# Optimization experiments

Measured on AMD Instinct MI355X. Metric: run time of the kernel, lower is better.

The kernel has to match this reference:

```python
import jax, jax.numpy as jnp
import numpy as np

K = 20
NEG_SLOPE = 0.2


def knn_idx(x, k):
    # squared euclidean pairwise distances [N, N]
    sq = jnp.sum(x * x, axis=-1)
    d = sq[:, None] - 2.0 * (x @ x.T) + sq[None, :]
    _, idx = jax.lax.top_k(-d, k)  # k nearest (self included, dist 0)
    return idx  # [N, k]


def edge_conv(x, W, b, k):
    # Dynamic EdgeConv: kNN on current features, gather, concat[x_i, x_j - x_i], MLP, max over neighbors
    idx = knn_idx(x, k)                 # [N, k]
    xj = x[idx]                         # [N, k, C] gather
    xi = jnp.broadcast_to(x[:, None, :], xj.shape)
    e = jnp.concatenate([xi, xj - xi], axis=-1)   # [N, k, 2C]
    h = jax.nn.leaky_relu(jnp.einsum('nkc,cf->nkf', e, W) + b, NEG_SLOPE)
    return jnp.max(h, axis=1)           # [N, F] max-aggregation


def setup_inputs() -> dict:
    key = jax.random.key(0)
    ks = jax.random.split(key, 7)
    N, C_in, H, F_out = 16384, 3, 64, 128
    def lin(k1, k2, fan_in, fan_out):
        lim = 1.0 / np.sqrt(fan_in)
        W = jax.random.uniform(k1, (fan_in, fan_out), jnp.float32, -lim, lim)
        b = jax.random.uniform(k2, (fan_out,), jnp.float32, -lim, lim)
        return W, b
    x = jax.random.normal(ks[0], (N, C_in), jnp.float32)
    W1, b1 = lin(ks[1], ks[2], 2 * C_in, H)
    W2, b2 = lin(ks[3], ks[4], 2 * H, H)
    W3, b3 = lin(ks[5], ks[6], 2 * H, F_out)
    return {"x": x, "W1": W1, "b1": b1, "W2": W2, "b2": b2, "W3": W3, "b3": b3}


def reference(x, W1, b1, W2, b2, W3, b3):
    h = edge_conv(x, W1, b1, K)
    h = edge_conv(h, W2, b2, K)
    h = edge_conv(h, W3, b3, K)
    return h
```

## Files before the change

kernel.cpp:

```cpp
#include <hip/hip_runtime.h>
#include <math.h>

#define K_NN 20
#define NEG_SLOPE 0.2f

constexpr int NSEG = 8;
constexpr int BKT  = 16;
constexpr int OCAP = 6144;

__device__ __forceinline__ void insert_sorted(float (&dl)[K_NN], int (&il)[K_NN],
                                              float d, int idx) {
    if (d < dl[K_NN - 1]) {
        dl[K_NN - 1] = d; il[K_NN - 1] = idx;
#pragma unroll
        for (int p = K_NN - 1; p > 0; --p) {
            if (dl[p] < dl[p - 1]) {
                float td = dl[p]; dl[p] = dl[p - 1]; dl[p - 1] = td;
                int   ti = il[p]; il[p] = il[p - 1]; il[p - 1] = ti;
            }
        }
    }
}

template<int C>
__global__ __launch_bounds__(256) void sqnorm_kernel(const float* __restrict__ x,
                                                     float* __restrict__ sq, int N) {
    int i = blockIdx.x * 256 + threadIdx.x;
    if (i < N) {
        float s = 0.f;
#pragma unroll
        for (int c = 0; c < C; ++c) { float v = x[i * C + c]; s += v * v; }
        sq[i] = s;
    }
}

__global__ __launch_bounds__(256) void pack3_kernel(const float* __restrict__ x,
                                                    float4* __restrict__ x4, int N) {
    int i = blockIdx.x * 256 + threadIdx.x;
    if (i < N) {
        float a = x[i * 3], b = x[i * 3 + 1], c = x[i * 3 + 2];
        float s = a * a; s += b * b; s += c * c;
        x4[i] = make_float4(a, b, c, s);
    }
}

__global__ __launch_bounds__(128) void tau3_kernel(const float4* __restrict__ x4,
                                                   float* __restrict__ tau, int N) {
    __shared__ float bufD[16 * 128];
    __shared__ int   bufI[16 * 128];
    const int tid = threadIdx.x;
    const int q   = blockIdx.x * 128 + tid;
    const float4 qv = x4[q];

    float dl[K_NN]; int il[K_NN];
#pragma unroll
    for (int p = 0; p < K_NN; ++p) { dl[p] = __builtin_inff(); il[p] = 0; }
    int cnt = 0;

    for (int j0 = 0; j0 < 2048; j0 += 8) {
#pragma unroll
        for (int u = 0; u < 8; ++u) {
            float4 pv = x4[j0 + u];
            float dot = qv.x * pv.x; dot += qv.y * pv.y; dot += qv.z * pv.z;
            float d = (qv.w - 2.f * dot) + pv.w;
            if (d < dl[K_NN - 1]) { bufD[tid + 128 * cnt] = d; bufI[tid + 128 * cnt] = j0 + u; ++cnt; }
        }
        if (__any(cnt >= 8)) {
            for (int u2 = 0; u2 < cnt; ++u2)
                insert_sorted(dl, il, bufD[tid + 128 * u2], bufI[tid + 128 * u2]);
            cnt = 0;
        }
    }
    for (int u2 = 0; u2 < cnt; ++u2)
        insert_sorted(dl, il, bufD[tid + 128 * u2], bufI[tid + 128 * u2]);

    tau[q] = dl[K_NN - 1] * 1.000002f + 2e-6f * qv.w;
}

__global__ __launch_bounds__(256) void knn3w_kernel(const float4* __restrict__ x4,
                                                    const float* __restrict__ tau,
                                                    float* __restrict__ pdist,
                                                    int* __restrict__ pidx, int N) {
    __shared__ float4 tile4[128];
    __shared__ float bufD[16 * 256];
    __shared__ int   bufI[16 * 256];
    const int tid = threadIdx.x;
    const int q   = blockIdx.x * 256 + tid;
    const int seg = blockIdx.y;
    const int segLen = N / NSEG;
    const int j0  = seg * segLen;

    const float4 qv = x4[q];
    const float  tq = tau[q];

    float dl[K_NN]; int il[K_NN];
#pragma unroll
    for (int p = 0; p < K_NN; ++p) { dl[p] = __builtin_inff(); il[p] = 0; }
    int cnt = 0;

    for (int t0 = 0; t0 < segLen; t0 += 128) {
        __syncthreads();
        if (tid < 128) tile4[tid] = x4[j0 + t0 + tid];
        __syncthreads();
        for (int jj = 0; jj < 128; jj += 8) {
#pragma unroll
            for (int u = 0; u < 8; ++u) {
                float4 pv = tile4[jj + u];
                float dot = qv.x * pv.x; dot += qv.y * pv.y; dot += qv.z * pv.z;
                float d = (qv.w - 2.f * dot) + pv.w;
                if (d <= tq && d < dl[K_NN - 1]) {
                    bufD[tid + 256 * cnt] = d;
                    bufI[tid + 256 * cnt] = j0 + t0 + jj + u;
                    ++cnt;
                }
            }
            if (__any(cnt >= 8)) {
                for (int u2 = 0; u2 < cnt; ++u2)
                    insert_sorted(dl, il, bufD[tid + 256 * u2], bufI[tid + 256 * u2]);
                cnt = 0;
            }
        }
    }
    for (int u2 = 0; u2 < cnt; ++u2)
        insert_sorted(dl, il, bufD[tid + 256 * u2], bufI[tid + 256 * u2]);

    const size_t base = ((size_t)q * NSEG + seg) * K_NN;
#pragma unroll
    for (int p = 0; p < K_NN; ++p) { pdist[base + p] = dl[p]; pidx[base + p] = il[p]; }
}

__global__ __launch_bounds__(256) void tau64_kernel(const float* __restrict__ feat,
                                                    const float* __restrict__ sq,
                                                    const int* __restrict__ knn,
                                                    float* __restrict__ tau, int N) {
    int q = blockIdx.x * 256 + threadIdx.x;
    if (q >= N) return;
    const float4* qrow = (const float4*)&feat[(size_t)q * 64];
    float4 qf[16];
#pragma unroll
    for (int m = 0; m < 16; ++m) qf[m] = qrow[m];
    const float qsq = sq[q];
    float t = 0.f;
    for (int k = 0; k < K_NN; ++k) {
        int j = knn[(size_t)q * K_NN + k];
        const float4* prow = (const float4*)&feat[(size_t)j * 64];
        float dot = 0.f;
#pragma unroll
        for (int m = 0; m < 16; ++m) {
            float4 pv = prow[m];
            dot += qf[m].x * pv.x; dot += qf[m].y * pv.y;
            dot += qf[m].z * pv.z; dot += qf[m].w * pv.w;
        }
        float d = (qsq - 2.f * dot) + sq[j];
        t = fmaxf(t, d);
    }
    tau[q] = t * 1.000002f + 2e-6f * qsq;
}

__global__ __launch_bounds__(256) void transpose64_kernel(const float* __restrict__ xin,
                                                          float* __restrict__ xT, int N) {
    int i = blockIdx.x * 256 + threadIdx.x;
    int c = blockIdx.y;
    xT[(size_t)c * N + i] = xin[(size_t)i * 64 + c];
}

__global__ __launch_bounds__(256, 2) void fused64s_kernel(const float* __restrict__ xT,
                                                          const float* __restrict__ sq,
                                                          const float* __restrict__ tau,
                                                          float* __restrict__ pdist,
                                                          int* __restrict__ pidx,
                                                          uint2* __restrict__ ovG, int N) {
    __shared__ float qT[64][132];
    __shared__ float pTc[2][8][140];
    __shared__ float qbufD[BKT][128];
    __shared__ int   qbufI[BKT][128];
    __shared__ float lstD[K_NN][128];
    __shared__ int   lstI[K_NN][128];
    __shared__ int   qn[128];
    __shared__ float thr_s[128];
    __shared__ int   ovf;
    __shared__ int   ovn;

    const int tid = threadIdx.x;
    const int q0  = blockIdx.x * 128;
    const int seg = blockIdx.y;
    const int segLen = N / NSEG;
    const int j0  = seg * segLen;
    uint2* ovBase = ovG + (size_t)(seg * gridDim.x + blockIdx.x) * OCAP;

    const int qg = tid >> 4, pg = tid & 15;
    const int qcol = qg * 8;
    const int pcol = pg * 8 + 4 * (pg >> 2);

#pragma unroll
    for (int k = 0; k < 8; ++k) {
        int v = tid + 256 * k; int c = v >> 5; int dd = (v & 31) * 4;
        *(float4*)&qT[c][dd] = *(const float4*)&xT[(size_t)c * N + q0 + dd];
    }
    float qsv[8];
    *(float4*)&qsv[0] = *(const float4*)&sq[q0 + qcol];
    *(float4*)&qsv[4] = *(const float4*)&sq[q0 + qcol + 4];
    float qtau[8];
    *(float4*)&qtau[0] = *(const float4*)&tau[q0 + qcol];
    *(float4*)&qtau[4] = *(const float4*)&tau[q0 + qcol + 4];

    if (tid < 128) {
        qn[tid] = 0; thr_s[tid] = __builtin_inff();
#pragma unroll
        for (int p = 0; p < K_NN; ++p) { lstD[p][tid] = __builtin_inff(); lstI[p][tid] = 0x7fffffff; }
    }
    if (tid == 0) { ovf = 0; ovn = 0; }

    const int stc  = tid >> 5;
    const int std_ = (tid & 31) * 4;
    const int sts  = std_ + 4 * (std_ >> 5);

    *(float4*)&pTc[0][stc][sts] = *(const float4*)&xT[(size_t)stc * N + j0 + std_];
    __syncthreads();

    int buf = 0;
    for (int t = 0; t < 16; ++t) {
        const int jb = j0 + t * 128;
        float acc[8][8];
#pragma unroll
        for (int i = 0; i < 8; ++i)
#pragma unroll
            for (int j = 0; j < 8; ++j) acc[i][j] = 0.f;

        for (int cc = 0; cc < 8; ++cc) {
            const bool last = (t == 15) && (cc == 7);
            float4 pnext;
            if (!last) {
                const int ncc = (cc + 1) & 7;
                const int njb = (cc == 7) ? jb + 128 : jb;
                pnext = *(const float4*)&xT[(size_t)(ncc * 8 + stc) * N + njb + std_];
            }
#pragma unroll
            for (int c8 = 0; c8 < 8; ++c8) {
                const int c = cc * 8 + c8;
                float4 qa  = *(const float4*)&qT[c][qcol];
                float4 qb4 = *(const float4*)&qT[c][qcol + 4];
                float4 pa  = *(const float4*)&pTc[buf][c8][pcol];
                float4 pb4 = *(const float4*)&pTc[buf][c8][pcol + 4];
                float qf[8] = {qa.x, qa.y, qa.z, qa.w, qb4.x, qb4.y, qb4.z, qb4.w};
                float pf[8] = {pa.x, pa.y, pa.z, pa.w, pb4.x, pb4.y, pb4.z, pb4.w};
#pragma unroll
                for (int i = 0; i < 8; ++i)
#pragma unroll
                    for (int j = 0; j < 8; ++j) acc[i][j] += qf[i] * pf[j];
            }
            if (!last) *(float4*)&pTc[buf ^ 1][stc][sts] = pnext;
            __syncthreads();
            buf ^= 1;
        }

        float psv[8];
        *(float4*)&psv[0] = *(const float4*)&sq[jb + pg * 8];
        *(float4*)&psv[4] = *(const float4*)&sq[jb + pg * 8 + 4];
        float thr_c[8];
#pragma unroll
        for (int i = 0; i < 8; ++i) thr_c[i] = thr_s[qcol + i];
        const int tbase = t * 128;

#pragma unroll
        for (int i = 0; i < 8; ++i) {
#pragma unroll
            for (int j = 0; j < 8; ++j) {
                float d = (qsv[i] - 2.f * acc[i][j]) + psv[j];
                if (d <= qtau[i] && d < thr_c[i]) {
                    int slot = atomicAdd(&qn[qcol + i], 1);
                    if (slot < BKT) {
                        qbufD[slot][qcol + i] = d;
                        qbufI[slot][qcol + i] = tbase + pg * 8 + j;
                    } else {
                        int os = atomicAdd(&ovn, 1);
                        if (os < OCAP)
                            ovBase[os] = make_uint2(__float_as_uint(d),
                                                    (unsigned)(((qcol + i) << 11) | (tbase + pg * 8 + j)));
                        ovf = 1;
                    }
                }
            }
        }
        __syncthreads();
        const int doDrain = ovf;
        __syncthreads();
        if (doDrain) {
            if (tid < 128) {
                int c = qn[tid]; c = (c < BKT) ? c : BKT;
                for (int s = 0; s < c; ++s) {
                    float d = qbufD[s][tid]; int idx = j0 + qbufI[s][tid];
                    float td = lstD[K_NN - 1][tid]; int ti = lstI[K_NN - 1][tid];
                    if (d < td || (d == td && idx < ti)) {
                        lstD[K_NN - 1][tid] = d; lstI[K_NN - 1][tid] = idx;
#pragma unroll
                        for (int p = K_NN - 1; p > 0; --p) {
                            float a = lstD[p][tid], b = lstD[p - 1][tid];
                            int  ai = lstI[p][tid], bi = lstI[p - 1][tid];
                            if (a < b || (a == b && ai < bi)) {
                                lstD[p][tid] = b; lstD[p - 1][tid] = a;
                                lstI[p][tid] = bi; lstI[p - 1][tid] = ai;
                            } else break;
                        }
                    }
                }
                qn[tid] = 0;
                thr_s[tid] = lstD[K_NN - 1][tid];
            }
            if (tid == 0) ovf = 0;
            __syncthreads();
        }
    }

    if (tid < 128) {
        int c = qn[tid]; c = (c < BKT) ? c : BKT;
        int tot = ovn; tot = (tot < OCAP) ? tot : OCAP;
        for (int s = 0; s < c + tot; ++s) {
            float d; int idx;
            if (s < c) { d = qbufD[s][tid]; idx = j0 + qbufI[s][tid]; }
            else {
                uint2 v = ovBase[s - c];
                if ((int)(v.y >> 11) != tid) continue;
                d = __uint_as_float(v.x); idx = j0 + (int)(v.y & 2047u);
            }
            float td = lstD[K_NN - 1][tid]; int ti = lstI[K_NN - 1][tid];
            if (d < td || (d == td && idx < ti)) {
                lstD[K_NN - 1][tid] = d; lstI[K_NN - 1][tid] = idx;
#pragma unroll
                for (int p = K_NN - 1; p > 0; --p) {
                    float a = lstD[p][tid], b = lstD[p - 1][tid];
                    int  ai = lstI[p][tid], bi = lstI[p - 1][tid];
                    if (a < b || (a == b && ai < bi)) {
                        lstD[p][tid] = b; lstD[p - 1][tid] = a;
                        lstI[p][tid] = bi; lstI[p - 1][tid] = ai;
                    } else break;
                }
            }
        }
        const size_t base = ((size_t)(q0 + tid) * NSEG + seg) * K_NN;
#pragma unroll
        for (int p = 0; p < K_NN; ++p) { pdist[base + p] = lstD[p][tid]; pidx[base + p] = lstI[p][tid]; }
    }
}

__global__ __launch_bounds__(256) void knn_merge_kernel(const float* __restrict__ pdist,
                                                        const int* __restrict__ pidx,
                                                        int* __restrict__ knn, int N) {
    int q = blockIdx.x * 256 + threadIdx.x;
    if (q >= N) return;
    float dl[K_NN]; int il[K_NN];
#pragma unroll
    for (int p = 0; p < K_NN; ++p) { dl[p] = __builtin_inff(); il[p] = 0; }

    for (int s = 0; s < NSEG; ++s) {
        const long base = ((long)q * NSEG + s) * K_NN;
        for (int p = 0; p < K_NN; ++p) {
            float d = pdist[base + p];
            if (!(d < dl[K_NN - 1])) break;
            insert_sorted(dl, il, d, pidx[base + p]);
        }
    }
#pragma unroll
    for (int p = 0; p < K_NN; ++p) knn[(long)q * K_NN + p] = il[p];
}

template<int C, int F>
__global__ __launch_bounds__(256) void proj_kernel(const float* __restrict__ x,
                                                   const float* __restrict__ W,
                                                   const float* __restrict__ b,
                                                   float* __restrict__ A,
                                                   float* __restrict__ U, int N) {
    int gid = blockIdx.x * 256 + threadIdx.x;
    int i = gid / F, f = gid % F;
    if (i >= N) return;
    float a = b[f], u = 0.f;
#pragma unroll
    for (int c = 0; c < C; ++c) {
        float xv = x[i * C + c];
        a += xv * W[c * F + f];
        u += xv * W[(C + c) * F + f];
    }
    A[(long)i * F + f] = a;
    U[(long)i * F + f] = u;
}

template<int F>
__global__ __launch_bounds__(256) void agg_kernel(const float* __restrict__ A,
                                                  const float* __restrict__ U,
                                                  const int* __restrict__ knn,
                                                  float* __restrict__ out, int N) {
    int gid = blockIdx.x * 256 + threadIdx.x;
    int i = gid / F, f = gid % F;
    if (i >= N) return;
    float a = A[(long)i * F + f] - U[(long)i * F + f];
    float m = -__builtin_inff();
#pragma unroll
    for (int k = 0; k < K_NN; ++k) {
        int j = knn[(long)i * K_NN + k];
        float v = a + U[(long)j * F + f];
        v = fmaxf(v, v * NEG_SLOPE);
        m = fmaxf(m, v);
    }
    out[(long)i * F + f] = m;
}

extern "C" void kernel_launch(void* const* d_in, const int* in_sizes, int n_in,
                              void* d_out, int out_size, void* d_ws, size_t ws_size,
                              hipStream_t stream) {
    const float* x  = (const float*)d_in[0];
    const float* W1 = (const float*)d_in[1];
    const float* b1 = (const float*)d_in[2];
    const float* W2 = (const float*)d_in[3];
    const float* b2 = (const float*)d_in[4];
    const float* W3 = (const float*)d_in[5];
    const float* b3 = (const float*)d_in[6];
    const int N = in_sizes[0] / 3;

    float* ws  = (float*)d_ws;
    float* sq  = ws;
    float* A   = sq + N;
    float* U   = A + (size_t)N * 128;
    float* h1  = U + (size_t)N * 128;
    float* h2  = h1 + (size_t)N * 64;
    float4* x4 = (float4*)(h2 + (size_t)N * 64);
    float* xT  = (float*)(x4 + N);
    float* tau = xT + (size_t)N * 64;
    float* pd  = tau + N;
    int* pidx  = (int*)(pd + (size_t)N * NSEG * K_NN);
    int* knn   = pidx + (size_t)N * NSEG * K_NN;
    uint2* ovG = (uint2*)(knn + (size_t)N * K_NN);
    float* out = (float*)d_out;

    const int qBlocks = N / 256;

    pack3_kernel<<<qBlocks, 256, 0, stream>>>(x, x4, N);
    tau3_kernel<<<N / 128, 128, 0, stream>>>(x4, tau, N);
    knn3w_kernel<<<dim3(qBlocks, NSEG), 256, 0, stream>>>(x4, tau, pd, pidx, N);
    knn_merge_kernel<<<qBlocks, 256, 0, stream>>>(pd, pidx, knn, N);
    proj_kernel<3, 64><<<(N * 64) / 256, 256, 0, stream>>>(x, W1, b1, A, U, N);
    agg_kernel<64><<<(N * 64) / 256, 256, 0, stream>>>(A, U, knn, h1, N);

    sqnorm_kernel<64><<<qBlocks, 256, 0, stream>>>(h1, sq, N);
    transpose64_kernel<<<dim3(qBlocks, 64), 256, 0, stream>>>(h1, xT, N);
    tau64_kernel<<<qBlocks, 256, 0, stream>>>(h1, sq, knn, tau, N);
    fused64s_kernel<<<dim3(N / 128, NSEG), 256, 0, stream>>>(xT, sq, tau, pd, pidx, ovG, N);
    knn_merge_kernel<<<qBlocks, 256, 0, stream>>>(pd, pidx, knn, N);
    proj_kernel<64, 64><<<(N * 64) / 256, 256, 0, stream>>>(h1, W2, b2, A, U, N);
    agg_kernel<64><<<(N * 64) / 256, 256, 0, stream>>>(A, U, knn, h2, N);

    sqnorm_kernel<64><<<qBlocks, 256, 0, stream>>>(h2, sq, N);
    transpose64_kernel<<<dim3(qBlocks, 64), 256, 0, stream>>>(h2, xT, N);
    tau64_kernel<<<qBlocks, 256, 0, stream>>>(h2, sq, knn, tau, N);
    fused64s_kernel<<<dim3(N / 128, NSEG), 256, 0, stream>>>(xT, sq, tau, pd, pidx, ovG, N);
    knn_merge_kernel<<<qBlocks, 256, 0, stream>>>(pd, pidx, knn, N);
    proj_kernel<64, 128><<<(N * 128) / 256, 256, 0, stream>>>(h2, W3, b3, A, U, N);
    agg_kernel<128><<<(N * 128) / 256, 256, 0, stream>>>(A, U, knn, out, N);
}
```

Before: 1.958 ms.

## Retile 64-dim kNN kernel to 32 queries per block and single-wave 3D kNN

The 64-channel fused distance/top-k kernel now handles 32 queries per block with 256 candidates per tile instead of 128x128. Each wave owns 8 queries and each lane 4 candidates, which cuts the accumulator from 8x8 to 8x4 and raises the occupancy target to 3 blocks. The 3D kNN kernel moves to 64-thread blocks that load their own tiles with no __syncthreads, relying on the single wave to stay in lockstep. The trade-off is lower arithmetic reuse per loaded element and a smaller overflow capacity (OCAP 2048), which could overflow sooner; 4x more blocks also increase per-block setup overhead.

```diff
diff --git a/kernel.cpp b/kernel.cpp
--- a/kernel.cpp
+++ b/kernel.cpp
@@ -4,9 +4,10 @@
 #define K_NN 20
 #define NEG_SLOPE 0.2f
 
-constexpr int NSEG = 8;
-constexpr int BKT  = 16;
-constexpr int OCAP = 6144;
+constexpr int NSEG1 = 8;
+constexpr int NSEG  = 8;
+constexpr int BKT   = 16;
+constexpr int OCAP  = 2048;
 
 __device__ __forceinline__ void insert_sorted(float (&dl)[K_NN], int (&il)[K_NN],
                                               float d, int idx) {
@@ -77,17 +78,17 @@
     tau[q] = dl[K_NN - 1] * 1.000002f + 2e-6f * qv.w;
 }
 
-__global__ __launch_bounds__(256) void knn3w_kernel(const float4* __restrict__ x4,
-                                                    const float* __restrict__ tau,
-                                                    float* __restrict__ pdist,
-                                                    int* __restrict__ pidx, int N) {
+__global__ __launch_bounds__(64) void knn3z_kernel(const float4* __restrict__ x4,
+                                                   const float* __restrict__ tau,
+                                                   float* __restrict__ pdist,
+                                                   int* __restrict__ pidx, int N) {
     __shared__ float4 tile4[128];
-    __shared__ float bufD[16 * 256];
-    __shared__ int   bufI[16 * 256];
-    const int tid = threadIdx.x;
-    const int q   = blockIdx.x * 256 + tid;
+    __shared__ float bufD[16 * 64];
+    __shared__ int   bufI[16 * 64];
+    const int t   = threadIdx.x;
+    const int q   = blockIdx.x * 64 + t;
     const int seg = blockIdx.y;
-    const int segLen = N / NSEG;
+    const int segLen = N / NSEG1;
     const int j0  = seg * segLen;
 
     const float4 qv = x4[q];
@@ -99,9 +100,8 @@
     int cnt = 0;
 
     for (int t0 = 0; t0 < segLen; t0 += 128) {
-        __syncthreads();
-        if (tid < 128) tile4[tid] = x4[j0 + t0 + tid];
-        __syncthreads();
+        tile4[t]      = x4[j0 + t0 + t];
+        tile4[t + 64] = x4[j0 + t0 + t + 64];
         for (int jj = 0; jj < 128; jj += 8) {
 #pragma unroll
             for (int u = 0; u < 8; ++u) {
@@ -109,22 +109,22 @@
                 float dot = qv.x * pv.x; dot += qv.y * pv.y; dot += qv.z * pv.z;
                 float d = (qv.w - 2.f * dot) + pv.w;
                 if (d <= tq && d < dl[K_NN - 1]) {
-                    bufD[tid + 256 * cnt] = d;
-                    bufI[tid + 256 * cnt] = j0 + t0 + jj + u;
+                    bufD[t + 64 * cnt] = d;
+                    bufI[t + 64 * cnt] = j0 + t0 + jj + u;
                     ++cnt;
                 }
             }
             if (__any(cnt >= 8)) {
                 for (int u2 = 0; u2 < cnt; ++u2)
-                    insert_sorted(dl, il, bufD[tid + 256 * u2], bufI[tid + 256 * u2]);
+                    insert_sorted(dl, il, bufD[t + 64 * u2], bufI[t + 64 * u2]);
                 cnt = 0;
             }
         }
     }
     for (int u2 = 0; u2 < cnt; ++u2)
-        insert_sorted(dl, il, bufD[tid + 256 * u2], bufI[tid + 256 * u2]);
-
-    const size_t base = ((size_t)q * NSEG + seg) * K_NN;
+        insert_sorted(dl, il, bufD[t + 64 * u2], bufI[t + 64 * u2]);
+
+    const size_t base = ((size_t)q * NSEG1 + seg) * K_NN;
 #pragma unroll
     for (int p = 0; p < K_NN; ++p) { pdist[base + p] = dl[p]; pidx[base + p] = il[p]; }
 }
@@ -164,119 +164,121 @@
     xT[(size_t)c * N + i] = xin[(size_t)i * 64 + c];
 }
 
-__global__ __launch_bounds__(256, 2) void fused64s_kernel(const float* __restrict__ xT,
+__global__ __launch_bounds__(256, 3) void fused64v_kernel(const float* __restrict__ xT,
                                                           const float* __restrict__ sq,
                                                           const float* __restrict__ tau,
                                                           float* __restrict__ pdist,
                                                           int* __restrict__ pidx,
                                                           uint2* __restrict__ ovG, int N) {
-    __shared__ float qT[64][132];
-    __shared__ float pTc[2][8][140];
-    __shared__ float qbufD[BKT][128];
-    __shared__ int   qbufI[BKT][128];
-    __shared__ float lstD[K_NN][128];
-    __shared__ int   lstI[K_NN][128];
-    __shared__ int   qn[128];
-    __shared__ float thr_s[128];
+    __shared__ float qT[64][36];
+    __shared__ float pT[2][8][256];
+    __shared__ float bktD[BKT][32];
+    __shared__ int   bktI[BKT][32];
+    __shared__ float lstD[K_NN][32];
+    __shared__ int   lstI[K_NN][32];
+    __shared__ int   qn[32];
+    __shared__ float thr_s[32];
     __shared__ int   ovf;
     __shared__ int   ovn;
 
-    const int tid = threadIdx.x;
-    const int q0  = blockIdx.x * 128;
-    const int seg = blockIdx.y;
+    const int tid  = threadIdx.x;
+    const int lane = tid & 63;
+    const int w    = tid >> 6;
+    const int q0   = blockIdx.x * 32;
+    const int seg  = blockIdx.y;
     const int segLen = N / NSEG;
-    const int j0  = seg * segLen;
-    uint2* ovBase = ovG + (size_t)(seg * gridDim.x + blockIdx.x) * OCAP;
-
-    const int qg = tid >> 4, pg = tid & 15;
-    const int qcol = qg * 8;
-    const int pcol = pg * 8 + 4 * (pg >> 2);
-
-#pragma unroll
-    for (int k = 0; k < 8; ++k) {
-        int v = tid + 256 * k; int c = v >> 5; int dd = (v & 31) * 4;
-        *(float4*)&qT[c][dd] = *(const float4*)&xT[(size_t)c * N + q0 + dd];
-    }
-    float qsv[8];
-    *(float4*)&qsv[0] = *(const float4*)&sq[q0 + qcol];
-    *(float4*)&qsv[4] = *(const float4*)&sq[q0 + qcol + 4];
-    float qtau[8];
-    *(float4*)&qtau[0] = *(const float4*)&tau[q0 + qcol];
-    *(float4*)&qtau[4] = *(const float4*)&tau[q0 + qcol + 4];
-
-    if (tid < 128) {
+    const int j0   = seg * segLen;
+    uint2* ovB = ovG + (size_t)(seg * gridDim.x + blockIdx.x) * OCAP;
+
+    const int rw = w * 2;
+    const int cl = lane * 4;
+
+    {
+        int c = tid >> 2, qq = (tid & 3) * 8;
+        *(float4*)&qT[c][qq]     = *(const float4*)&xT[(size_t)c * N + q0 + qq];
+        *(float4*)&qT[c][qq + 4] = *(const float4*)&xT[(size_t)c * N + q0 + qq + 4];
+    }
+    if (tid < 32) {
         qn[tid] = 0; thr_s[tid] = __builtin_inff();
 #pragma unroll
         for (int p = 0; p < K_NN; ++p) { lstD[p][tid] = __builtin_inff(); lstI[p][tid] = 0x7fffffff; }
     }
     if (tid == 0) { ovf = 0; ovn = 0; }
 
-    const int stc  = tid >> 5;
-    const int std_ = (tid & 31) * 4;
-    const int sts  = std_ + 4 * (std_ >> 5);
-
-    *(float4*)&pTc[0][stc][sts] = *(const float4*)&xT[(size_t)stc * N + j0 + std_];
+    float qsv[8], qtau[8], thr_c[8];
+    *(float4*)&qsv[0]  = *(const float4*)&sq[q0 + w * 8];
+    *(float4*)&qsv[4]  = *(const float4*)&sq[q0 + w * 8 + 4];
+    *(float4*)&qtau[0] = *(const float4*)&tau[q0 + w * 8];
+    *(float4*)&qtau[4] = *(const float4*)&tau[q0 + w * 8 + 4];
+#pragma unroll
+    for (int i = 0; i < 8; ++i) thr_c[i] = __builtin_inff();
+
+    {
+        float4 a = *(const float4*)&xT[(size_t)(rw)     * N + j0 + cl];
+        float4 b = *(const float4*)&xT[(size_t)(rw + 1) * N + j0 + cl];
+        *(float4*)&pT[0][rw][cl]     = a;
+        *(float4*)&pT[0][rw + 1][cl] = b;
+    }
     __syncthreads();
 
+    const int nT = segLen / 256;
     int buf = 0;
-    for (int t = 0; t < 16; ++t) {
-        const int jb = j0 + t * 128;
-        float acc[8][8];
+    for (int t = 0; t < nT; ++t) {
+        const int jb = j0 + t * 256;
+        float acc[8][4];
 #pragma unroll
         for (int i = 0; i < 8; ++i)
 #pragma unroll
-            for (int j = 0; j < 8; ++j) acc[i][j] = 0.f;
+            for (int j = 0; j < 4; ++j) acc[i][j] = 0.f;
 
         for (int cc = 0; cc < 8; ++cc) {
-            const bool last = (t == 15) && (cc == 7);
-            float4 pnext;
+            const bool last = (t == nT - 1) && (cc == 7);
+            float4 na, nb;
             if (!last) {
                 const int ncc = (cc + 1) & 7;
-                const int njb = (cc == 7) ? jb + 128 : jb;
-                pnext = *(const float4*)&xT[(size_t)(ncc * 8 + stc) * N + njb + std_];
+                const int njb = (cc == 7) ? jb + 256 : jb;
+                na = *(const float4*)&xT[(size_t)(ncc * 8 + rw)     * N + njb + cl];
+                nb = *(const float4*)&xT[(size_t)(ncc * 8 + rw + 1) * N + njb + cl];
             }
 #pragma unroll
             for (int c8 = 0; c8 < 8; ++c8) {
                 const int c = cc * 8 + c8;
-                float4 qa  = *(const float4*)&qT[c][qcol];
-                float4 qb4 = *(const float4*)&qT[c][qcol + 4];
-                float4 pa  = *(const float4*)&pTc[buf][c8][pcol];
-                float4 pb4 = *(const float4*)&pTc[buf][c8][pcol + 4];
-                float qf[8] = {qa.x, qa.y, qa.z, qa.w, qb4.x, qb4.y, qb4.z, qb4.w};
-                float pf[8] = {pa.x, pa.y, pa.z, pa.w, pb4.x, pb4.y, pb4.z, pb4.w};
+                float4 qa = *(const float4*)&qT[c][w * 8];
+                float4 qb = *(const float4*)&qT[c][w * 8 + 4];
+                float4 pv = *(const float4*)&pT[buf][c8][cl];
+                float qf[8] = {qa.x, qa.y, qa.z, qa.w, qb.x, qb.y, qb.z, qb.w};
+                float pf[4] = {pv.x, pv.y, pv.z, pv.w};
 #pragma unroll
                 for (int i = 0; i < 8; ++i)
 #pragma unroll
-                    for (int j = 0; j < 8; ++j) acc[i][j] += qf[i] * pf[j];
-            }
-            if (!last) *(float4*)&pTc[buf ^ 1][stc][sts] = pnext;
+                    for (int j = 0; j < 4; ++j) acc[i][j] += qf[i] * pf[j];
+            }
+            if (!last) {
+                *(float4*)&pT[buf ^ 1][rw][cl]     = na;
+                *(float4*)&pT[buf ^ 1][rw + 1][cl] = nb;
+            }
             __syncthreads();
             buf ^= 1;
         }
 
-        float psv[8];
-        *(float4*)&psv[0] = *(const float4*)&sq[jb + pg * 8];
-        *(float4*)&psv[4] = *(const float4*)&sq[jb + pg * 8 + 4];
-        float thr_c[8];
-#pragma unroll
-        for (int i = 0; i < 8; ++i) thr_c[i] = thr_s[qcol + i];
-        const int tbase = t * 128;
-
+        float psv[4];
+        *(float4*)&psv[0] = *(const float4*)&sq[jb + cl];
+        const int tbase = t * 256;
 #pragma unroll
         for (int i = 0; i < 8; ++i) {
 #pragma unroll
-            for (int j = 0; j < 8; ++j) {
+            for (int j = 0; j < 4; ++j) {
                 float d = (qsv[i] - 2.f * acc[i][j]) + psv[j];
                 if (d <= qtau[i] && d < thr_c[i]) {
-                    int slot = atomicAdd(&qn[qcol + i], 1);
+                    int slot = atomicAdd(&qn[w * 8 + i], 1);
                     if (slot < BKT) {
-                        qbufD[slot][qcol + i] = d;
-                        qbufI[slot][qcol + i] = tbase + pg * 8 + j;
+                        bktD[slot][w * 8 + i] = d;
+                        bktI[slot][w * 8 + i] = tbase + cl + j;
                     } else {
                         int os = atomicAdd(&ovn, 1);
                         if (os < OCAP)
-                            ovBase[os] = make_uint2(__float_as_uint(d),
-                                                    (unsigned)(((qcol + i) << 11) | (tbase + pg * 8 + j)));
+                            ovB[os] = make_uint2(__float_as_uint(d),
+                                (unsigned)(((w * 8 + i) << 11) | (tbase + cl + j)));
                         ovf = 1;
                     }
                 }
@@ -286,10 +288,10 @@
         const int doDrain = ovf;
         __syncthreads();
         if (doDrain) {
-            if (tid < 128) {
+            if (tid < 32) {
                 int c = qn[tid]; c = (c < BKT) ? c : BKT;
                 for (int s = 0; s < c; ++s) {
-                    float d = qbufD[s][tid]; int idx = j0 + qbufI[s][tid];
+                    float d = bktD[s][tid]; int idx = j0 + bktI[s][tid];
                     float td = lstD[K_NN - 1][tid]; int ti = lstI[K_NN - 1][tid];
                     if (d < td || (d == td && idx < ti)) {
                         lstD[K_NN - 1][tid] = d; lstI[K_NN - 1][tid] = idx;
@@ -310,16 +312,18 @@
             if (tid == 0) ovf = 0;
             __syncthreads();
         }
-    }
-
-    if (tid < 128) {
+#pragma unroll
+        for (int i = 0; i < 8; ++i) thr_c[i] = thr_s[w * 8 + i];
+    }
+
+    if (tid < 32) {
         int c = qn[tid]; c = (c < BKT) ? c : BKT;
         int tot = ovn; tot = (tot < OCAP) ? tot : OCAP;
         for (int s = 0; s < c + tot; ++s) {
             float d; int idx;
-            if (s < c) { d = qbufD[s][tid]; idx = j0 + qbufI[s][tid]; }
+            if (s < c) { d = bktD[s][tid]; idx = j0 + bktI[s][tid]; }
             else {
-                uint2 v = ovBase[s - c];
+                uint2 v = ovB[s - c];
                 if ((int)(v.y >> 11) != tid) continue;
                 d = __uint_as_float(v.x); idx = j0 + (int)(v.y & 2047u);
             }
@@ -345,15 +349,16 @@
 
 __global__ __launch_bounds__(256) void knn_merge_kernel(const float* __restrict__ pdist,
                                                         const int* __restrict__ pidx,
-                                                        int* __restrict__ knn, int N) {
+                                                        int* __restrict__ knn,
+                                                        int N, int nseg) {
     int q = blockIdx.x * 256 + threadIdx.x;
     if (q >= N) return;
     float dl[K_NN]; int il[K_NN];
 #pragma unroll
     for (int p = 0; p < K_NN; ++p) { dl[p] = __builtin_inff(); il[p] = 0; }
 
-    for (int s = 0; s < NSEG; ++s) {
-        const long base = ((long)q * NSEG + s) * K_NN;
+    for (int s = 0; s < nseg; ++s) {
+        const long base = ((long)q * nseg + s) * K_NN;
         for (int p = 0; p < K_NN; ++p) {
             float d = pdist[base + p];
             if (!(d < dl[K_NN - 1])) break;
@@ -426,8 +431,8 @@
     float* xT  = (float*)(x4 + N);
     float* tau = xT + (size_t)N * 64;
     float* pd  = tau + N;
-    int* pidx  = (int*)(pd + (size_t)N * NSEG * K_NN);
-    int* knn   = pidx + (size_t)N * NSEG * K_NN;
+    int* pidx  = (int*)(pd + (size_t)N * NSEG1 * K_NN);
+    int* knn   = pidx + (size_t)N * NSEG1 * K_NN;
     uint2* ovG = (uint2*)(knn + (size_t)N * K_NN);
     float* out = (float*)d_out;
 
@@ -435,24 +440,24 @@
 
     pack3_kernel<<<qBlocks, 256, 0, stream>>>(x, x4, N);
     tau3_kernel<<<N / 128, 128, 0, stream>>>(x4, tau, N);
-    knn3w_kernel<<<dim3(qBlocks, NSEG), 256, 0, stream>>>(x4, tau, pd, pidx, N);
-    knn_merge_kernel<<<qBlocks, 256, 0, stream>>>(pd, pidx, knn, N);
+    knn3z_kernel<<<dim3(N / 64, NSEG1), 64, 0, stream>>>(x4, tau, pd, pidx, N);
+    knn_merge_kernel<<<qBlocks, 256, 0, stream>>>(pd, pidx, knn, N, NSEG1);
     proj_kernel<3, 64><<<(N * 64) / 256, 256, 0, stream>>>(x, W1, b1, A, U, N);
     agg_kernel<64><<<(N * 64) / 256, 256, 0, stream>>>(A, U, knn, h1, N);
 
     sqnorm_kernel<64><<<qBlocks, 256, 0, stream>>>(h1, sq, N);
     transpose64_kernel<<<dim3(qBlocks, 64), 256, 0, stream>>>(h1, xT, N);
     tau64_kernel<<<qBlocks, 256, 0, stream>>>(h1, sq, knn, tau, N);
-    fused64s_kernel<<<dim3(N / 128, NSEG), 256, 0, stream>>>(xT, sq, tau, pd, pidx, ovG, N);
-    knn_merge_kernel<<<qBlocks, 256, 0, stream>>>(pd, pidx, knn, N);
+    fused64v_kernel<<<dim3(N / 32, NSEG), 256, 0, stream>>>(xT, sq, tau, pd, pidx, ovG, N);
+    knn_merge_kernel<<<qBlocks, 256, 0, stream>>>(pd, pidx, knn, N, NSEG);
     proj_kernel<64, 64><<<(N * 64) / 256, 256, 0, stream>>>(h1, W2, b2, A, U, N);
     agg_kernel<64><<<(N * 64) / 256, 256, 0, stream>>>(A, U, knn, h2, N);
 
     sqnorm_kernel<64><<<qBlocks, 256, 0, stream>>>(h2, sq, N);
     transpose64_kernel<<<dim3(qBlocks, 64), 256, 0, stream>>>(h2, xT, N);
     tau64_kernel<<<qBlocks, 256, 0, stream>>>(h2, sq, knn, tau, N);
-    fused64s_kernel<<<dim3(N / 128, NSEG), 256, 0, stream>>>(xT, sq, tau, pd, pidx, ovG, N);
-    knn_merge_kernel<<<qBlocks, 256, 0, stream>>>(pd, pidx, knn, N);
+    fused64v_kernel<<<dim3(N / 32, NSEG), 256, 0, stream>>>(xT, sq, tau, pd, pidx, ovG, N);
+    knn_merge_kernel<<<qBlocks, 256, 0, stream>>>(pd, pidx, knn, N, NSEG);
     proj_kernel<64, 128><<<(N * 128) / 256, 256, 0, stream>>>(h2, W3, b3, A, U, N);
     agg_kernel<128><<<(N * 128) / 256, 256, 0, stream>>>(A, U, knn, out, N);
 }
```

New measurement: 2.758 ms. +40.8%, slower.
